# Kernel optimization log

Hardware: AMD Instinct MI355X
Metric: run time of the kernel (lower is better)

Reference implementation:

```python
import jax, jax.numpy as jnp
import numpy as np
from jax import lax

N = 200; E = 3200; HID = 64; NH = 16; OUT = 2 * HID; CAT = NH * OUT  # CAT = 2048
ALPHA = 0.2


def _gat(h, e_attr, adj, n2n, W, a_s, a_d, a_e, We, concat):
    # edge-feature-aware GAT head: logits from Wh_i, Wh_j and projected node2node feats
    Nn = h.shape[0]
    Wh = h @ W                                       # [N, out]
    ee = ((n2n @ We) @ a_e).reshape(Nn, Nn)          # [N, N] edge-feature term
    logits = jax.nn.leaky_relu((Wh @ a_s)[:, None] + (Wh @ a_d)[None, :] + ee,
                               negative_slope=ALPHA)
    logits = jnp.where(adj > 0, logits, -1e9)        # mask to graph structure
    att = jax.nn.softmax(logits, axis=1)
    h2 = att @ Wh
    if concat:
        h2 = jax.nn.elu(h2)
    return h2, jax.nn.elu(e_attr @ We)               # updated node + edge features


def _edge_pool(x, eidx, e, w, b):
    # static-shape edge pooling: score edges, gate nodes by mean incident score
    src, dst = eidx[0], eidx[1]
    s = jax.nn.sigmoid(jnp.concatenate([x[src], x[dst], e], axis=1) @ w + b)  # [E]
    deg = jax.ops.segment_sum(jnp.ones_like(s), src, num_segments=x.shape[0])
    ns = jax.ops.segment_sum(s, src, num_segments=x.shape[0]) / (deg + 1e-6)
    return x * ns[:, None], e * s[:, None]


def _gpool(x, w, b):
    # GlobalAttention: gate_nn = Linear+Sigmoid, softmax over nodes, weighted sum
    gate = jax.nn.softmax(jax.nn.sigmoid(x @ w + b), axis=0)  # [N, 1]
    return jnp.sum(gate * x, axis=0, keepdims=True)           # [1, D]


def _adj_n2n(Nn, eidx, eattr):
    # vectorized version of the per-edge Python loop in _get_adj_node2node
    src, dst = eidx[0], eidx[1]
    adj = jnp.zeros((Nn, Nn), eattr.dtype).at[src, dst].set(1.0)
    n2n = jnp.zeros((Nn * Nn, eattr.shape[1]), eattr.dtype).at[src * Nn + dst].set(eattr)
    return adj, n2n


def _lstm_dir(x, Wih, Whh, b):
    # one LSTM direction over seq x [T, Din] (PyTorch i,f,g,o gate order)
    Hh = Whh.shape[1]
    def step(carry, xt):
        h, c = carry
        g = xt @ Wih.T + h @ Whh.T + b
        i, f, gg, o = jnp.split(g, 4)
        c = jax.nn.sigmoid(f) * c + jax.nn.sigmoid(i) * jnp.tanh(gg)
        h = jax.nn.sigmoid(o) * jnp.tanh(c)
        return (h, c), h
    (_, _), ys = lax.scan(step, (jnp.zeros(Hh, x.dtype), jnp.zeros(Hh, x.dtype)), x)
    return ys


def setup_inputs():
    key = jax.random.key(0)
    ks = iter(jax.random.split(key, 64))
    def rn(shape, scale=0.05):
        return jax.random.normal(next(ks), shape, jnp.float32) * scale
    inp = {}
    for g in (1, 2):
        eidx = jax.random.randint(next(ks), (2, E), 0, N)
        eattr = rn((E, HID), 1.0)
        adj, n2n = _adj_n2n(N, eidx, eattr)
        inp['features%d' % g] = rn((N, HID), 1.0)
        inp['edge_index%d' % g] = eidx
        inp['edgesAttr%d' % g] = eattr
        inp['adjacency%d' % g] = adj
        inp['node2node%d' % g] = n2n
    inp.update(dict(
        W_h=rn((HID, HID)),
        W_gat=rn((NH, HID, OUT)), a_src=rn((NH, OUT)), a_dst=rn((NH, OUT)),
        a_e=rn((NH, OUT)), We_gat=rn((NH, HID, OUT)),
        W_out=rn((CAT, OUT)), ao_src=rn((OUT,)), ao_dst=rn((OUT,)), ao_e=rn((OUT,)),
        We_out=rn((CAT, OUT)),
        ep1_w=rn((3 * CAT,)), ep1_b=rn(()),
        ep2_w=rn((3 * OUT,)), ep2_b=rn(()),
        g1_w=rn((HID, 1)), g1_b=rn((1,)),
        g2_w=rn((CAT, 1)), g2_b=rn((1,)),
        g3_w=rn((OUT, 1)), g3_b=rn((1,)),
        Wih0=rn((2, 512, 35 * HID)), Whh0=rn((2, 512, 128)), b0=rn((2, 512)),
        Wih1=rn((2, 512, 256)), Whh1=rn((2, 512, 128)), b1=rn((2, 512)),
        fc_w=rn((256, 2)), fc_b=rn((2,)),
    ))
    return inp


def reference(features1, features2, edge_index1, edge_index2, edgesAttr1, edgesAttr2,
              adjacency1, adjacency2, node2node1, node2node2,
              W_h, W_gat, a_src, a_dst, a_e, We_gat,
              W_out, ao_src, ao_dst, ao_e, We_out,
              ep1_w, ep1_b, ep2_w, ep2_b,
              g1_w, g1_b, g2_w, g2_b, g3_w, g3_b,
              Wih0, Whh0, b0, Wih1, Whh1, b1, fc_w, fc_b):
    def graph(feat, eidx, eattr, adj, n2n):
        h = jax.nn.elu(feat @ W_h)                              # SingleNodeAttentionLayer
        hs = [_gpool(h, g1_w, g1_b)]
        outs = [_gat(h, eattr, adj, n2n, W_gat[i], a_src[i], a_dst[i], a_e[i],
                     We_gat[i], True) for i in range(NH)]
        h = jnp.concatenate([o[0] for o in outs], axis=1)       # [N, 2048]
        eattr = jnp.concatenate([o[1] for o in outs], axis=1)   # [E, 2048]
        h, eattr = _edge_pool(h, eidx, eattr, ep1_w, ep1_b)
        hs.append(_gpool(h, g2_w, g2_b))
        adj2, n2n2 = _adj_n2n(h.shape[0], eidx, eattr)          # dense [N*N, 2048]
        h, eattr = _gat(h, eattr, adj2, n2n2, W_out, ao_src, ao_dst, ao_e, We_out, False)
        h, eattr = _edge_pool(h, eidx, eattr, ep2_w, ep2_b)
        hs.append(_gpool(h, g3_w, g3_b))
        return jnp.concatenate(hs, axis=1)                      # [1, 35*HID]

    h1 = graph(features1, edge_index1, edgesAttr1, adjacency1, node2node1)
    h2 = graph(features2, edge_index2, edgesAttr2, adjacency2, node2node2)
    x = jnp.concatenate([h1, h2], axis=0)                       # seq [2, 2240]
    for Wih, Whh, b in ((Wih0, Whh0, b0), (Wih1, Whh1, b1)):
        f = _lstm_dir(x, Wih[0], Whh[0], b[0])
        r = _lstm_dir(x[::-1], Wih[1], Whh[1], b[1])[::-1]
        x = jnp.concatenate([f, r], axis=1)                     # [2, 256]
    logits = x[-1] @ fc_w + fc_b
    return jax.nn.softmax(logits)[None, :]                      # [1, nclass]
```

## Files before the change

kernel.cpp:

```cpp
#include <hip/hip_runtime.h>
#include <math.h>

#define DI static __device__ __forceinline__

DI float eluf(float x){ return x > 0.f ? x : expm1f(x); }
DI float lreluf(float x){ return x > 0.f ? x : 0.2f*x; }
DI float sigmf(float x){ return 1.f/(1.f+expf(-x)); }

typedef unsigned short u16;
typedef unsigned int   u32;
typedef __attribute__((ext_vector_type(8))) short short8_t;
typedef __attribute__((ext_vector_type(4))) float f32x4;

DI u16 bf16rne(float f){
  u32 u = __float_as_uint(f);
  u += 0x7fffu + ((u>>16)&1u);
  return (u16)(u>>16);
}

DI f32x4 bmfma(short8_t a, short8_t b, f32x4 c){
  return __builtin_amdgcn_mfma_f32_16x16x32_bf16(a, b, c, 0, 0, 0);
}

constexpr int N=200, E=3200, HID=64, NH=16, OUTD=128, CAT=2048, SEQD=2240;

constexpr int OH0   = 0;
constexpr int OWH   = OH0 + N*HID;
constexpr int OASN  = OWH + NH*N*OUTD;
constexpr int OADN  = OASN + NH*N;
constexpr int OH1   = OADN + NH*N;
constexpr int OXW1  = OH1 + N*CAT;
constexpr int OXW2  = OXW1 + 256;
constexpr int OEW1  = OXW2 + 256;
constexpr int OS1   = OEW1 + E;
constexpr int ODEG1 = OS1 + E;
constexpr int OSS1  = ODEG1 + 256;
constexpr int ORAW1 = OSS1 + 256;
constexpr int OWH2  = ORAW1 + 256;
constexpr int OAS2  = OWH2 + N*OUTD;
constexpr int OAD2  = OAS2 + 256;
constexpr int OEWV  = OAD2 + 256;
constexpr int OH2B  = OEWV + E;
constexpr int OXS2  = OH2B + N*OUTD;
constexpr int OXD2  = OXS2 + 256;
constexpr int ODEG2 = OXD2 + 256;
constexpr int OSS2  = ODEG2 + 256;
constexpr int ORAW2 = OSS2 + 256;
constexpr int ORAW3 = ORAW2 + 256;
constexpr int PGF   = ORAW3 + 256;
constexpr int GLOBF = 10624;
constexpr int TOTF  = GLOBF + 2*PGF;

__device__ __attribute__((aligned(16))) float G_F[TOTF];
__device__ float G_E2PART[(size_t)4*2*E*OUTD];
__device__ float G_EDOTH[2*NH*E];
__device__ float G_WHHT[2*2*128*512];
__device__ int   G_PIDX[2*N*N];
__device__ __attribute__((aligned(16))) u16 G_WGAT_T[NH*OUTD*HID];
__device__ __attribute__((aligned(16))) u16 G_WOUT_T[OUTD*CAT];
__device__ __attribute__((aligned(16))) u16 G_EATTR_BF[2*E*HID];

DI float* gf(int g){ return G_F + GLOBF + (size_t)g*PGF; }
DI float* gwe_ae(){ return G_F; }
DI float* gv_e(){ return G_F + 1024; }
DI float* gy0(){ return G_F + 3072; }
DI float* gy1(){ return G_F + 3584; }
DI float* gxseq(){ return G_F + 4096; }
DI float* gxg(){ return G_F + 8576; }
DI int*   gpidx(int g){ return G_PIDX + g*N*N; }

struct GraphIn {
  const float *feat, *eattr, *adj, *n2n;
  const int   *eidx;
};

struct Params {
  GraphIn g[2];
  const float *W_h, *W_gat, *a_src, *a_dst, *a_e, *We_gat;
  const float *W_out, *ao_src, *ao_dst, *ao_e, *We_out;
  const float *ep1_w, *ep1_b, *ep2_w, *ep2_b;
  const float *g1_w, *g1_b, *g2_w, *g2_b, *g3_w, *g3_b;
  const float *Wih0, *Whh0, *b0, *Wih1, *Whh1, *b1, *fc_w, *fc_b;
  float *out;
};

constexpr int ZPG  = 2*E + 1024;
constexpr int IB_Z = (2*ZPG+255)/256;
constexpr int IB_C = (2*N*N+255)/256;
constexpr int IB_D = (2*2*512*128)/256;
constexpr int IB_E = (NH*HID+CAT+3)/4;
constexpr int IB_H = (2*N+3)/4;
constexpr int IB_W1 = (NH*OUTD*HID)/256;
constexpr int IB_W2 = (OUTD*CAT)/256;
constexpr int IB_EA = (2*E*HID)/256;
__global__ void k_init(Params P){
  int b = blockIdx.x, tid = threadIdx.x;
  if (b < IB_Z){
    int i = b*256 + tid;
    if (i < 2*ZPG){
      int g = i/ZPG, r = i%ZPG;
      int addr = r<E ? OEW1+r : (r<2*E ? OEWV+(r-E) :
                 (r<2*E+512 ? ODEG1+(r-2*E) : ODEG2+(r-2*E-512)));
      gf(g)[addr] = 0.f;
    }
  } else if (b < IB_Z+IB_C){
    int i = (b-IB_Z)*256 + tid; if (i < 2*N*N) G_PIDX[i] = -1;
  } else if (b < IB_Z+IB_C+IB_D){
    int idx = (b-IB_Z-IB_C)*256 + tid;
    int l = idx >> 17;
    int r = idx & 131071;
    int d = r >> 16;
    int r2 = r & 65535;
    int gate = r2 & 511;
    int k = r2 >> 9;
    const float* Whh = l ? P.Whh1 : P.Whh0;
    G_WHHT[idx] = Whh[((size_t)d*512+gate)*128 + k];
  } else if (b < IB_Z+IB_C+IB_D+IB_E){
    int gid = (b-IB_Z-IB_C-IB_D)*4 + (tid>>6);
    int lane = tid & 63;
    if (gid < NH*HID){
      int h = gid/HID, c = gid%HID;
      const float* W = P.We_gat + (size_t)(h*HID+c)*OUTD;
      const float* a = P.a_e + h*OUTD;
      float acc = 0.f;
      for (int o=lane;o<OUTD;o+=64) acc += W[o]*a[o];
      for (int off=32;off>0;off>>=1) acc += __shfl_down(acc,off);
      if (lane==0) gwe_ae()[gid] = acc;
    } else if (gid < NH*HID+CAT){
      int c = gid - NH*HID;
      const float* W = P.We_out + (size_t)c*OUTD;
      float acc = 0.f;
      for (int o=lane;o<OUTD;o+=64) acc += W[o]*P.ao_e[o];
      for (int off=32;off>0;off>>=1) acc += __shfl_down(acc,off);
      if (lane==0) gv_e()[c] = acc;
    }
  } else if (b < IB_Z+IB_C+IB_D+IB_E+IB_H){
    int unit = (b-IB_Z-IB_C-IB_D-IB_E)*4 + (tid>>6);
    if (unit >= 2*N) return;
    int g = unit / N, n = unit % N, c = tid & 63;
    const float* feat = P.g[g].feat;
    float acc = 0.f;
    for (int k=0;k<HID;k++) acc += feat[n*HID+k]*P.W_h[k*HID+c];
    float v = eluf(acc);
    float* f = gf(g);
    f[OH0 + n*HID + c] = v;
    float r = v*P.g1_w[c];
    for (int off=32;off>0;off>>=1) r += __shfl_down(r,off);
    if (c==0) f[ORAW1+n] = r;
  } else if (b < IB_Z+IB_C+IB_D+IB_E+IB_H+IB_W1){
    int i = (b-(IB_Z+IB_C+IB_D+IB_E+IB_H))*256 + tid;
    int h = i>>13, o = (i>>6)&127, c = i&63;
    G_WGAT_T[i] = bf16rne(P.We_gat[(size_t)(h*HID+c)*OUTD + o]);
  } else if (b < IB_Z+IB_C+IB_D+IB_E+IB_H+IB_W1+IB_W2){
    int i = (b-(IB_Z+IB_C+IB_D+IB_E+IB_H+IB_W1))*256 + tid;
    int n = i>>11, q = i&2047;
    G_WOUT_T[i] = bf16rne(P.We_out[(size_t)q*OUTD + n]);
  } else {
    int i = (b-(IB_Z+IB_C+IB_D+IB_E+IB_H+IB_W1+IB_W2))*256 + tid;
    int g = i >= E*HID ? 1 : 0;
    G_EATTR_BF[i] = bf16rne(P.g[g].eattr[i - g*E*HID]);
  }
}
constexpr int IB_TOT = IB_Z+IB_C+IB_D+IB_E+IB_H+IB_W1+IB_W2+IB_EA;


DI void e2p_body(Params& P, int idx, char* smem){
  int g = idx/400, r2 = idx%400, hg = r2/100, eb = r2%100;
  int tid = threadIdx.x;
  int wave = tid>>6, lane = tid&63, l16 = lane&15, l4 = lane>>4;
  u16* Tlds = (u16*)smem;
  int e0 = eb*32;
  int nt0 = wave*2;
  const u16* ea = G_EATTR_BF + ((size_t)g*E + e0)*HID;
  short8_t af00 = *(const short8_t*)(ea + l16*HID + l4*8);
  short8_t af01 = *(const short8_t*)(ea + l16*HID + 32 + l4*8);
  short8_t af10 = *(const short8_t*)(ea + (16+l16)*HID + l4*8);
  short8_t af11 = *(const short8_t*)(ea + (16+l16)*HID + 32 + l4*8);
  float ew1p0[4] = {0.f,0.f,0.f,0.f}, ewvp0[4] = {0.f,0.f,0.f,0.f};
  float ew1p1[4] = {0.f,0.f,0.f,0.f}, ewvp1[4] = {0.f,0.f,0.f,0.f};
  for (int hh=0; hh<4; hh++){
    int h = hg*4 + hh;
    const u16* Wg = G_WGAT_T + (size_t)h*OUTD*HID;
    #pragma unroll
    for (int nn=0; nn<2; nn++){
      int nt = nt0 + nn;
      const u16* Wgn = Wg + (size_t)(nt*16 + l16)*HID + l4*8;
      short8_t wg0 = *(const short8_t*)Wgn;
      short8_t wg1 = *(const short8_t*)(Wgn + 32);
      f32x4 d0 = {0.f,0.f,0.f,0.f}, d1 = {0.f,0.f,0.f,0.f};
      d0 = bmfma(af00, wg0, d0);
      d1 = bmfma(af10, wg0, d1);
      d0 = bmfma(af01, wg1, d0);
      d1 = bmfma(af11, wg1, d1);
      int qg = h*OUTD + nt*16 + l16;
      float w1 = P.ep1_w[2*CAT + qg];
      float wv = gv_e()[qg];
      int qloc = hh*128 + nt*16 + l16;
      #pragma unroll
      for (int r=0;r<4;r++){
        float v0 = d0[r] > 0.f ? d0[r] : expm1f(d0[r]);
        float v1 = d1[r] > 0.f ? d1[r] : expm1f(d1[r]);
        ew1p0[r] += v0*w1; ewvp0[r] += v0*wv;
        ew1p1[r] += v1*w1; ewvp1[r] += v1*wv;
        int row = l4*4 + r;
        int byt = (row*1024 + qloc*2) ^ ((row&7)<<4);
        *(u16*)((char*)Tlds + byt) = bf16rne(v0);
        *(u16*)((char*)Tlds + byt + 16384) = bf16rne(v1);
      }
    }
  }
  const u16* WoA = G_WOUT_T + (size_t)(wave*32 + l16)*CAT + hg*512 + l4*8;
  const u16* WoB = WoA + 16*CAT;
  short8_t w0a = *(const short8_t*)WoA;
  short8_t w0b = *(const short8_t*)WoB;
  short8_t w1a = *(const short8_t*)(WoA + 32);
  short8_t w1b = *(const short8_t*)(WoB + 32);
  float* f = gf(g);
  #pragma unroll
  for (int r=0;r<4;r++){
    float a0 = ew1p0[r], b0 = ewvp0[r], a1 = ew1p1[r], b1 = ewvp1[r];
    a0 += __shfl_xor(a0,1); b0 += __shfl_xor(b0,1); a1 += __shfl_xor(a1,1); b1 += __shfl_xor(b1,1);
    a0 += __shfl_xor(a0,2); b0 += __shfl_xor(b0,2); a1 += __shfl_xor(a1,2); b1 += __shfl_xor(b1,2);
    a0 += __shfl_xor(a0,4); b0 += __shfl_xor(b0,4); a1 += __shfl_xor(a1,4); b1 += __shfl_xor(b1,4);
    a0 += __shfl_xor(a0,8); b0 += __shfl_xor(b0,8); a1 += __shfl_xor(a1,8); b1 += __shfl_xor(b1,8);
    if (l16==0){
      int e = e0 + l4*4 + r;
      atomicAdd(&f[OEW1+e], a0);
      atomicAdd(&f[OEWV+e], b0);
      atomicAdd(&f[OEW1+e+16], a1);
      atomicAdd(&f[OEWV+e+16], b1);
    }
  }
  __syncthreads();
  f32x4 acc00 = {0.f,0.f,0.f,0.f}, acc01 = {0.f,0.f,0.f,0.f};
  f32x4 acc10 = {0.f,0.f,0.f,0.f}, acc11 = {0.f,0.f,0.f,0.f};
  #pragma unroll
  for (int ks=0; ks<16; ks++){
    short8_t na = w0a, nb = w0b;
    if (ks < 14){
      na = *(const short8_t*)(WoA + (ks+2)*32);
      nb = *(const short8_t*)(WoB + (ks+2)*32);
    }
    int byt = (l16*1024 + ks*64 + l4*16) ^ ((l16&7)<<4);
    short8_t a0 = *(const short8_t*)((const char*)Tlds + byt);
    short8_t a1 = *(const short8_t*)((const char*)Tlds + byt + 16384);
    acc00 = bmfma(a0, w0a, acc00);
    acc10 = bmfma(a1, w0a, acc10);
    acc01 = bmfma(a0, w0b, acc01);
    acc11 = bmfma(a1, w0b, acc11);
    w0a = w1a; w0b = w1b; w1a = na; w1b = nb;
  }
  float* dst = G_E2PART + (((size_t)hg*2 + g)*E + e0)*OUTD;
  #pragma unroll
  for (int r=0;r<4;r++){
    int ee = l4*4 + r;
    dst[(size_t)ee*OUTD + wave*32 + l16]      = acc00[r];
    dst[(size_t)ee*OUTD + wave*32 + 16 + l16] = acc01[r];
    dst[(size_t)(16+ee)*OUTD + wave*32 + l16]      = acc10[r];
    dst[(size_t)(16+ee)*OUTD + wave*32 + 16 + l16] = acc11[r];
  }
}

DI void edoth_body(Params& P, int idx, float* s){
  int tid = threadIdx.x;
  int g = idx / (E/16);
  int e0 = (idx % (E/16)) * 16;
  float (*ea)[HID+1] = (float(*)[HID+1])s;
  float (*wa)[HID+1] = (float(*)[HID+1])(s + 16*(HID+1));
  {
    int row = tid >> 4, c0 = (tid & 15)*4;
    float4 v = *(const float4*)&P.g[g].eattr[(size_t)(e0+row)*HID + c0];
    ea[row][c0]=v.x; ea[row][c0+1]=v.y; ea[row][c0+2]=v.z; ea[row][c0+3]=v.w;
    float4 w = *(const float4*)&gwe_ae()[row*HID + c0];
    wa[row][c0]=w.x; wa[row][c0+1]=w.y; wa[row][c0+2]=w.z; wa[row][c0+3]=w.w;
  }
  __syncthreads();
  int h = tid >> 4, el = tid & 15;
  float acc = 0.f;
  #pragma unroll
  for (int c=0;c<HID;c++) acc += ea[el][c]*wa[h][c];
  G_EDOTH[((size_t)g*NH + h)*E + e0 + el] = acc;
}

DI void wh_body(Params& P, int idx, float* s){
  int o = threadIdx.x;
  if (o >= 128) return;
  int g = idx / (N*(NH+1));
  int r = idx % (N*(NH+1));
  int h = r / N, n = r % N;
  float* f = gf(g);
  if (h == NH){
    if (n != 0) return;
    float* att = s;
    float* sb  = s + 200;
    for (int j = o; j < N; j += 128) att[j] = sigmf(f[ORAW1+j] + P.g1_b[0]);
    __syncthreads();
    float m = -3e38f;
    for (int j = o; j < N; j += 128) m = fmaxf(m, att[j]);
    sb[o] = m; __syncthreads();
    for (int sft=64;sft>0;sft>>=1){ if (o<sft) sb[o]=fmaxf(sb[o],sb[o+sft]); __syncthreads(); }
    m = sb[0]; __syncthreads();
    float ss = 0.f;
    for (int j = o; j < N; j += 128){ float e = expf(att[j]-m); ss += e; }
    sb[o] = ss; __syncthreads();
    for (int sft=64;sft>0;sft>>=1){ if (o<sft) sb[o]+=sb[o+sft]; __syncthreads(); }
    float inv = 1.f/sb[0]; __syncthreads();
    for (int j = o; j < N; j += 128) att[j] = expf(att[j]-m)*inv;
    __syncthreads();
    if (o < HID){
      float acc = 0.f;
      for (int j=0;j<N;j++) acc += att[j]*f[OH0 + j*HID + o];
      gxseq()[g*SEQD + o] = acc;
    }
    return;
  }
  float* hs   = s;
  float* sred = s + 64;
  float* dred = s + 192;
  if (o < HID) hs[o] = f[OH0 + n*HID + o];
  __syncthreads();
  const float* W = P.W_gat + (size_t)h*HID*OUTD + o;
  float acc = 0.f;
  for (int c=0;c<HID;c++) acc += hs[c]*W[(size_t)c*OUTD];
  f[OWH + ((size_t)h*N + n)*OUTD + o] = acc;
  sred[o] = acc*P.a_src[h*OUTD+o];
  dred[o] = acc*P.a_dst[h*OUTD+o];
  __syncthreads();
  for (int sft=64;sft>0;sft>>=1){ if (o<sft){ sred[o]+=sred[o+sft]; dred[o]+=dred[o+sft]; } __syncthreads(); }
  if (o==0){ f[OASN+h*N+n]=sred[0]; f[OADN+h*N+n]=dred[0]; }
}

DI void pairs_body(Params& P, int idx){
  int g = idx / 13;
  int e = (idx % 13)*256 + threadIdx.x;
  if (e >= E) return;
  const int* ei = P.g[g].eidx;
  atomicMax(&gpidx(g)[ei[e]*N + ei[E+e]], e);
}

constexpr int MB_E2P = 800, MB_ED = 400, MB_WH = 2*N*(NH+1), MB_PR = 26;
__global__ __launch_bounds__(256) void k_mega(Params P){
  __shared__ __attribute__((aligned(16))) char smem[32768];
  int b = blockIdx.x;
  if (b < MB_E2P) e2p_body(P, b, smem);
  else if (b < MB_E2P+MB_ED) edoth_body(P, b-MB_E2P, (float*)smem);
  else if (b < MB_E2P+MB_ED+MB_WH) wh_body(P, b-(MB_E2P+MB_ED), (float*)smem);
  else pairs_body(P, b-(MB_E2P+MB_ED+MB_WH));
}

__global__ void k_att1(Params P){
  int nb = blockIdx.x, h = blockIdx.y, g = blockIdx.z, tid = threadIdx.x;
  int n0 = nb*4;
  __shared__ float z[4][N];
  __shared__ float red[128];
  __shared__ float sinv[4];
  float* f = gf(g);
  const float* adj = P.g[g].adj;
  const int* pidx = gpidx(g);
  const float* edoth = G_EDOTH + ((size_t)g*NH + h)*E;
  const float* adn = f + OADN + h*N;
  for (int i=0;i<4;i++){
    float asn = f[OASN + h*N + n0+i];
    for (int j = tid; j < N; j += 128){
      float a = adj[(n0+i)*N + j];
      float zz;
      if (a > 0.f){
        int p = pidx[(n0+i)*N + j];
        float ee = (p >= 0) ? edoth[p] : 0.f;
        zz = lreluf(asn + adn[j] + ee);
      } else zz = -1e9f;
      z[i][j] = zz;
    }
  }
  __syncthreads();
  for (int i=0;i<4;i++){
    float m = -3e38f;
    for (int j = tid; j < N; j += 128) m = fmaxf(m, z[i][j]);
    red[tid] = m; __syncthreads();
    for (int s=64;s>0;s>>=1){ if (tid<s) red[tid]=fmaxf(red[tid],red[tid+s]); __syncthreads(); }
    m = red[0]; __syncthreads();
    float ssum = 0.f;
    for (int j = tid; j < N; j += 128){ float e = expf(z[i][j]-m); z[i][j]=e; ssum += e; }
    red[tid] = ssum; __syncthreads();
    for (int s=64;s>0;s>>=1){ if (tid<s) red[tid]+=red[tid+s]; __syncthreads(); }
    if (tid==0) sinv[i] = 1.f/red[0];
    __syncthreads();
  }
  const float* wh = f + OWH + (size_t)h*N*OUTD;
  float a0=0.f,a1=0.f,a2=0.f,a3=0.f;
  for (int j=0;j<N;j++){
    float w = wh[(size_t)j*OUTD + tid];
    a0 += z[0][j]*w; a1 += z[1][j]*w; a2 += z[2][j]*w; a3 += z[3][j]*w;
  }
  f[OH1 + (size_t)(n0+0)*CAT + h*OUTD + tid] = eluf(a0*sinv[0]);
  f[OH1 + (size_t)(n0+1)*CAT + h*OUTD + tid] = eluf(a1*sinv[1]);
  f[OH1 + (size_t)(n0+2)*CAT + h*OUTD + tid] = eluf(a2*sinv[2]);
  f[OH1 + (size_t)(n0+3)*CAT + h*OUTD + tid] = eluf(a3*sinv[3]);
}

__global__ void k_xw1(Params P){
  int n = blockIdx.x, g = blockIdx.y, tid = threadIdx.x;
  __shared__ float s1b[256], s2b[256], s3b[256];
  float* f = gf(g);
  const float* x = f + OH1 + (size_t)n*CAT;
  float a1 = 0.f, a2 = 0.f, a3 = 0.f;
  for (int c = tid; c < CAT; c += 256){
    float xv = x[c];
    a1 += xv*P.ep1_w[c];
    a2 += xv*P.ep1_w[CAT+c];
    a3 += xv*P.g2_w[c];
  }
  s1b[tid]=a1; s2b[tid]=a2; s3b[tid]=a3; __syncthreads();
  for (int s=128;s>0;s>>=1){
    if (tid<s){ s1b[tid]+=s1b[tid+s]; s2b[tid]+=s2b[tid+s]; s3b[tid]+=s3b[tid+s]; }
    __syncthreads();
  }
  if (tid==0){ f[OXW1+n]=s1b[0]; f[OXW2+n]=s2b[0]; f[ORAW2+n]=s3b[0]; }
}

__global__ void k_s1(Params P){
  int e = blockIdx.x*256 + threadIdx.x, g = blockIdx.y;
  if (e >= E) return;
  float* f = gf(g);
  const int* ei = P.g[g].eidx;
  int s = ei[e], d = ei[E+e];
  float v = sigmf(f[OXW1+s] + f[OXW2+d] + f[OEW1+e] + P.ep1_b[0]);
  f[OS1+e] = v;
  atomicAdd(&f[OSS1+s], v);
  atomicAdd(&f[ODEG1+s], 1.f);
}

DI void gpool_body(Params& P, int xoff, int D, int odeg, int rawoff,
                   const float* bb, int outoff, int cb, int g,
                   float* att, float* sb){
  int tid = threadIdx.x;
  float* f = gf(g);
  if (tid < N){
    float sc = f[odeg+256+tid]/(f[odeg+tid]+1e-6f);
    att[tid] = sigmf(f[rawoff+tid]*sc + bb[0]);
  }
  __syncthreads();
  float m = (tid < N) ? att[tid] : -3e38f;
  sb[tid] = m; __syncthreads();
  for (int s=256;s>0;s>>=1){ if (tid<s) sb[tid]=fmaxf(sb[tid],sb[tid+s]); __syncthreads(); }
  m = sb[0]; __syncthreads();
  float e = (tid < N) ? expf(att[tid]-m) : 0.f;
  sb[tid] = e; __syncthreads();
  for (int s=256;s>0;s>>=1){ if (tid<s) sb[tid]+=sb[tid+s]; __syncthreads(); }
  float inv = 1.f/sb[0]; __syncthreads();
  if (tid < N){
    float sc = f[odeg+256+tid]/(f[odeg+tid]+1e-6f);
    att[tid] = e*inv*sc;
  }
  __syncthreads();
  int c = cb*512 + tid;
  if (c < D){
    const float* x = f + xoff;
    float acc = 0.f;
    for (int n=0;n<N;n++) acc += att[n]*x[(size_t)n*D + c];
    gxseq()[g*SEQD + outoff + c] = acc;
  }
}

__global__ void k_gpools(Params P){
  __shared__ float att[N];
  __shared__ float sb[512];
  int b = blockIdx.x;
  if (b < 8){
    int g = b >> 2, cb = b & 3;
    gpool_body(P, OH1, CAT, ODEG1, ORAW2, P.g2_b, HID, cb, g, att, sb);
  } else {
    int g = b - 8;
    gpool_body(P, OH2B, OUTD, ODEG2, ORAW3, P.g3_b, HID+CAT, 0, g, att, sb);
  }
}

__global__ void k_Wh2(Params P){
  int n = blockIdx.x, g = blockIdx.y, tid = threadIdx.x;
  int kq = tid >> 7, o = tid & 127;
  __shared__ float hrow[4][128];
  __shared__ float part[4][128];
  __shared__ float sr[128], dr[128];
  float* f = gf(g);
  const float* x = f + OH1 + (size_t)n*CAT;
  float acc = 0.f;
  for (int cc=0; cc<4; cc++){
    int c0 = kq*512 + cc*128;
    __syncthreads();
    hrow[kq][o] = x[c0 + o];
    __syncthreads();
    const float* W = P.W_out + (size_t)c0*OUTD + o;
    for (int j=0;j<128;j++) acc += hrow[kq][j]*W[(size_t)j*OUTD];
  }
  part[kq][o] = acc;
  __syncthreads();
  if (kq==0){
    float ns = f[OSS1+n]/(f[ODEG1+n]+1e-6f);
    float a = part[0][o]+part[1][o]+part[2][o]+part[3][o];
    float v = a*ns;
    f[OWH2 + (size_t)n*OUTD + o] = v;
    sr[o] = v*P.ao_src[o];
    dr[o] = v*P.ao_dst[o];
  }
  __syncthreads();
  for (int s=64;s>0;s>>=1){
    if (tid<s){ sr[tid]+=sr[tid+s]; dr[tid]+=dr[tid+s]; }
    __syncthreads();
  }
  if (tid==0){ f[OAS2+n]=sr[0]; f[OAD2+n]=dr[0]; }
}

__global__ void k_att2(Params P){
  int n = blockIdx.x, g = blockIdx.y, tid = threadIdx.x;
  __shared__ float z[N];
  __shared__ float red[128];
  __shared__ float dred[128];
  __shared__ float gred[128];
  float* f = gf(g);
  const float* adj = P.g[g].adj;
  const int* pidx = gpidx(g);
  float asn = f[OAS2+n];
  const float* adn = f + OAD2;
  for (int j = tid; j < N; j += 128){
    float a = adj[n*N + j];
    float zz;
    if (a > 0.f){
      int p = pidx[n*N + j];
      float ee = (p >= 0) ? f[OEWV+p]*f[OS1+p] : 0.f;
      zz = lreluf(asn + adn[j] + ee);
    } else zz = -1e9f;
    z[j] = zz;
  }
  __syncthreads();
  float m = -3e38f;
  for (int j = tid; j < N; j += 128) m = fmaxf(m, z[j]);
  red[tid] = m; __syncthreads();
  for (int s=64;s>0;s>>=1){ if (tid<s) red[tid]=fmaxf(red[tid],red[tid+s]); __syncthreads(); }
  m = red[0]; __syncthreads();
  float ssum = 0.f;
  for (int j = tid; j < N; j += 128){ float e = expf(z[j]-m); z[j]=e; ssum += e; }
  red[tid] = ssum; __syncthreads();
  for (int s=64;s>0;s>>=1){ if (tid<s) red[tid]+=red[tid+s]; __syncthreads(); }
  float inv = 1.f/red[0]; __syncthreads();
  const float* wh = f + OWH2;
  float acc = 0.f;
  for (int j=0;j<N;j++){
    float w = z[j];
    if (w != 0.f) acc += w * wh[(size_t)j*OUTD + tid];
  }
  float v = acc*inv;
  f[OH2B + (size_t)n*OUTD + tid] = v;
  red[tid]  = v*P.ep2_w[tid];
  dred[tid] = v*P.ep2_w[OUTD+tid];
  gred[tid] = v*P.g3_w[tid];
  __syncthreads();
  for (int s=64;s>0;s>>=1){
    if (tid<s){ red[tid]+=red[tid+s]; dred[tid]+=dred[tid+s]; gred[tid]+=gred[tid+s]; }
    __syncthreads();
  }
  if (tid==0){ f[OXS2+n]=red[0]; f[OXD2+n]=dred[0]; f[ORAW3+n]=gred[0]; }
}

constexpr int TE2 = 16;
__global__ void k_ew2fin(Params P){
  int e0 = blockIdx.x*TE2, g = blockIdx.y, tid = threadIdx.x;
  __shared__ float lred[2][TE2];
  float* f = gf(g);
  float w2 = P.ep2_w[2*OUTD + tid];
  int lane = tid & 63, wvi = tid >> 6;
  for (int e=0;e<TE2;e++){
    const float* src = G_E2PART + ((size_t)g*E + e0 + e)*OUTD + tid;
    float a = 0.f;
    #pragma unroll
    for (int h=0;h<4;h++) a += src[(size_t)h*2*E*OUTD];
    float v = eluf(f[OS1+e0+e]*a) * w2;
    for (int off=32;off>0;off>>=1) v += __shfl_down(v,off);
    if (lane==0) lred[wvi][e]=v;
  }
  __syncthreads();
  if (tid < TE2){
    int e = e0 + tid;
    float ew2 = lred[0][tid]+lred[1][tid];
    const int* ei = P.g[g].eidx;
    int s = ei[e], d = ei[E+e];
    float v = sigmf(f[OXS2+s] + f[OXD2+d] + ew2 + P.ep2_b[0]);
    atomicAdd(&f[OSS2+s], v);
    atomicAdd(&f[ODEG2+s], 1.f);
  }
}

__global__ void k_lstm_xg(Params P, int layer){
  int gid = blockIdx.x*4 + (threadIdx.x>>6);
  int lane = threadIdx.x & 63;
  int t = gid >> 10;
  int rem = gid & 1023;
  int d = rem >> 9;
  int gate = rem & 511;
  const float* Wih = layer ? P.Wih1 : P.Wih0;
  const float* bb  = layer ? P.b1   : P.b0;
  const float* xin = layer ? gy0()  : gxseq();
  int Din = layer ? 256 : SEQD;
  const float* x = xin + t*Din;
  const float* Wr = Wih + ((size_t)d*512 + gate)*Din;
  float acc = 0.f;
  for (int k=lane; k<Din; k+=64) acc += x[k]*Wr[k];
  for (int off=32; off>0; off>>=1) acc += __shfl_down(acc, off);
  if (lane==0) gxg()[(t*2 + d)*512 + gate] = acc + bb[d*512 + gate];
}

__global__ void k_lstm_rec(Params P, int layer){
  int d = blockIdx.x, tid = threadIdx.x;
  float* yout = layer ? gy1() : gy0();
  const float* T = G_WHHT + (size_t)(layer*2 + d)*128*512;
  __shared__ float h[128], c[128], gbuf[512];
  if (tid < 128){ h[tid]=0.f; c[tid]=0.f; }
  __syncthreads();
  for (int s=0;s<2;s++){
    int t = (d==0) ? s : 1-s;
    float acc = gxg()[(t*2 + d)*512 + tid];
    for (int k=0;k<128;k++) acc += h[k]*T[(size_t)k*512 + tid];
    gbuf[tid] = acc;
    __syncthreads();
    if (tid < 128){
      float ii = sigmf(gbuf[tid]);
      float ff = sigmf(gbuf[128+tid]);
      float gg = tanhf(gbuf[256+tid]);
      float oo = sigmf(gbuf[384+tid]);
      float cn = ff*c[tid] + ii*gg;
      c[tid] = cn;
      float hn = oo*tanhf(cn);
      h[tid] = hn;
      yout[t*256 + d*128 + tid] = hn;
    }
    __syncthreads();
  }
}

__global__ void k_final(Params P){
  int tid = threadIdx.x;
  __shared__ float sb[256], sb2[256];
  const float* x = gy1() + 256;
  sb[tid]  = x[tid]*P.fc_w[tid*2+0];
  sb2[tid] = x[tid]*P.fc_w[tid*2+1];
  __syncthreads();
  for (int s=128;s>0;s>>=1){ if (tid<s){ sb[tid]+=sb[tid+s]; sb2[tid]+=sb2[tid+s]; } __syncthreads(); }
  if (tid==0){
    float l0 = sb[0] + P.fc_b[0];
    float l1 = sb2[0] + P.fc_b[1];
    float m = fmaxf(l0,l1);
    float e0 = expf(l0-m), e1 = expf(l1-m), inv = 1.f/(e0+e1);
    P.out[0] = e0*inv;
    P.out[1] = e1*inv;
  }
}

extern "C" void kernel_launch(void* const* d_in, const int* in_sizes, int n_in,
                              void* d_out, int out_size, void* d_ws, size_t ws_size,
                              hipStream_t stream){
  Params P;
  for (int g=0; g<2; ++g){
    int b = g*5;
    P.g[g].feat  = (const float*)d_in[b+0];
    P.g[g].eidx  = (const int*)d_in[b+1];
    P.g[g].eattr = (const float*)d_in[b+2];
    P.g[g].adj   = (const float*)d_in[b+3];
    P.g[g].n2n   = (const float*)d_in[b+4];
  }
  P.W_h   = (const float*)d_in[10];
  P.W_gat = (const float*)d_in[11];
  P.a_src = (const float*)d_in[12];
  P.a_dst = (const float*)d_in[13];
  P.a_e   = (const float*)d_in[14];
  P.We_gat= (const float*)d_in[15];
  P.W_out = (const float*)d_in[16];
  P.ao_src= (const float*)d_in[17];
  P.ao_dst= (const float*)d_in[18];
  P.ao_e  = (const float*)d_in[19];
  P.We_out= (const float*)d_in[20];
  P.ep1_w = (const float*)d_in[21];
  P.ep1_b = (const float*)d_in[22];
  P.ep2_w = (const float*)d_in[23];
  P.ep2_b = (const float*)d_in[24];
  P.g1_w  = (const float*)d_in[25];
  P.g1_b  = (const float*)d_in[26];
  P.g2_w  = (const float*)d_in[27];
  P.g2_b  = (const float*)d_in[28];
  P.g3_w  = (const float*)d_in[29];
  P.g3_b  = (const float*)d_in[30];
  P.Wih0  = (const float*)d_in[31];
  P.Whh0  = (const float*)d_in[32];
  P.b0    = (const float*)d_in[33];
  P.Wih1  = (const float*)d_in[34];
  P.Whh1  = (const float*)d_in[35];
  P.b1    = (const float*)d_in[36];
  P.fc_w  = (const float*)d_in[37];
  P.fc_b  = (const float*)d_in[38];
  P.out   = (float*)d_out;

  k_init <<<dim3(IB_TOT), 256, 0, stream>>>(P);
  k_mega <<<dim3(MB_E2P+MB_ED+MB_WH+MB_PR), 256, 0, stream>>>(P);
  k_att1 <<<dim3(N/4,NH,2),128, 0, stream>>>(P);
  k_xw1  <<<dim3(N,2),    256, 0, stream>>>(P);
  k_s1   <<<dim3((E+255)/256,2), 256, 0, stream>>>(P);
  k_Wh2  <<<dim3(N,2),    512, 0, stream>>>(P);
  k_att2 <<<dim3(N,2),    128, 0, stream>>>(P);
  k_ew2fin<<<dim3(E/TE2,2),128, 0, stream>>>(P);
  k_gpools<<<dim3(10),    512, 0, stream>>>(P);

  k_lstm_xg <<<dim3(512), 256, 0, stream>>>(P, 0);
  k_lstm_rec<<<dim3(2),   512, 0, stream>>>(P, 0);
  k_lstm_xg <<<dim3(512), 256, 0, stream>>>(P, 1);
  k_lstm_rec<<<dim3(2),   512, 0, stream>>>(P, 1);
  k_final<<<dim3(1), 256, 0, stream>>>(P);
}
```

Measured before the change: 338.3 us.

## Fuse post-attention stages into fewer kernels and merge LSTM layer-1 with final FC

Folds the per-node projection reductions (k_xw1) into the attention kernel's epilogue, accumulated with atomics into zeroed buffers. Merges the s1 edge scoring with a 4-node-per-block Wh2 projection, and att2 with the first global pool. It also moves the node-score scaling algebraically from Wh2 into att2, and fuses the second LSTM recurrence with the final FC/softmax into one 1024-thread block. The aim is to cut launch count and serial kernel boundaries in a latency-bound pipeline, at the cost of atomics and larger shared-memory blocks.

```diff
diff --git a/kernel.cpp b/kernel.cpp
--- a/kernel.cpp
+++ b/kernel.cpp
@@ -84,7 +84,7 @@
   float *out;
 };
 
-constexpr int ZPG  = 2*E + 1024;
+constexpr int ZPG  = 2*E + 1024 + 768;
 constexpr int IB_Z = (2*ZPG+255)/256;
 constexpr int IB_C = (2*N*N+255)/256;
 constexpr int IB_D = (2*2*512*128)/256;
@@ -99,8 +99,14 @@
     int i = b*256 + tid;
     if (i < 2*ZPG){
       int g = i/ZPG, r = i%ZPG;
-      int addr = r<E ? OEW1+r : (r<2*E ? OEWV+(r-E) :
-                 (r<2*E+512 ? ODEG1+(r-2*E) : ODEG2+(r-2*E-512)));
+      int addr;
+      if (r < E) addr = OEW1+r;
+      else if (r < 2*E) addr = OEWV+(r-E);
+      else if (r < 2*E+512) addr = ODEG1+(r-2*E);
+      else if (r < 2*E+1024) addr = ODEG2+(r-2*E-512);
+      else if (r < 2*E+1280) addr = OXW1+(r-2*E-1024);
+      else if (r < 2*E+1536) addr = OXW2+(r-2*E-1280);
+      else addr = ORAW2+(r-2*E-1536);
       gf(g)[addr] = 0.f;
     }
   } else if (b < IB_Z+IB_C){
@@ -354,6 +360,7 @@
   __shared__ float z[4][N];
   __shared__ float red[128];
   __shared__ float sinv[4];
+  __shared__ float lxr[2][12];
   float* f = gf(g);
   const float* adj = P.g[g].adj;
   const int* pidx = gpidx(g);
@@ -392,34 +399,99 @@
     float w = wh[(size_t)j*OUTD + tid];
     a0 += z[0][j]*w; a1 += z[1][j]*w; a2 += z[2][j]*w; a3 += z[3][j]*w;
   }
-  f[OH1 + (size_t)(n0+0)*CAT + h*OUTD + tid] = eluf(a0*sinv[0]);
-  f[OH1 + (size_t)(n0+1)*CAT + h*OUTD + tid] = eluf(a1*sinv[1]);
-  f[OH1 + (size_t)(n0+2)*CAT + h*OUTD + tid] = eluf(a2*sinv[2]);
-  f[OH1 + (size_t)(n0+3)*CAT + h*OUTD + tid] = eluf(a3*sinv[3]);
-}
-
-__global__ void k_xw1(Params P){
-  int n = blockIdx.x, g = blockIdx.y, tid = threadIdx.x;
-  __shared__ float s1b[256], s2b[256], s3b[256];
+  float v0 = eluf(a0*sinv[0]);
+  float v1 = eluf(a1*sinv[1]);
+  float v2 = eluf(a2*sinv[2]);
+  float v3 = eluf(a3*sinv[3]);
+  f[OH1 + (size_t)(n0+0)*CAT + h*OUTD + tid] = v0;
+  f[OH1 + (size_t)(n0+1)*CAT + h*OUTD + tid] = v1;
+  f[OH1 + (size_t)(n0+2)*CAT + h*OUTD + tid] = v2;
+  f[OH1 + (size_t)(n0+3)*CAT + h*OUTD + tid] = v3;
+  float w1 = P.ep1_w[h*OUTD + tid];
+  float w2 = P.ep1_w[CAT + h*OUTD + tid];
+  float w3 = P.g2_w[h*OUTD + tid];
+  float pp[12];
+  pp[0]=v0*w1; pp[1]=v0*w2; pp[2]=v0*w3;
+  pp[3]=v1*w1; pp[4]=v1*w2; pp[5]=v1*w3;
+  pp[6]=v2*w1; pp[7]=v2*w2; pp[8]=v2*w3;
+  pp[9]=v3*w1; pp[10]=v3*w2; pp[11]=v3*w3;
+  #pragma unroll
+  for (int k=0;k<12;k++){
+    #pragma unroll
+    for (int off=32;off>0;off>>=1) pp[k] += __shfl_down(pp[k],off);
+  }
+  int wv = tid>>6, ln = tid&63;
+  if (ln==0){
+    #pragma unroll
+    for (int k=0;k<12;k++) lxr[wv][k]=pp[k];
+  }
+  __syncthreads();
+  if (tid<12){
+    float s = lxr[0][tid]+lxr[1][tid];
+    int node = n0 + tid/3, kind = tid%3;
+    int base = kind==0 ? OXW1 : (kind==1 ? OXW2 : ORAW2);
+    atomicAdd(&f[base + node], s);
+  }
+}
+
+DI void wh2_body(Params& P, int nq, int g, char* smem){
+  float* hrow = (float*)smem;
+  float* part = (float*)(smem + 32768);
+  float* lred = (float*)(smem + 32768 + 8192);
+  int tid = threadIdx.x;
   float* f = gf(g);
-  const float* x = f + OH1 + (size_t)n*CAT;
-  float a1 = 0.f, a2 = 0.f, a3 = 0.f;
-  for (int c = tid; c < CAT; c += 256){
-    float xv = x[c];
-    a1 += xv*P.ep1_w[c];
-    a2 += xv*P.ep1_w[CAT+c];
-    a3 += xv*P.g2_w[c];
-  }
-  s1b[tid]=a1; s2b[tid]=a2; s3b[tid]=a3; __syncthreads();
-  for (int s=128;s>0;s>>=1){
-    if (tid<s){ s1b[tid]+=s1b[tid+s]; s2b[tid]+=s2b[tid+s]; s3b[tid]+=s3b[tid+s]; }
-    __syncthreads();
-  }
-  if (tid==0){ f[OXW1+n]=s1b[0]; f[OXW2+n]=s2b[0]; f[ORAW2+n]=s3b[0]; }
-}
-
-__global__ void k_s1(Params P){
-  int e = blockIdx.x*256 + threadIdx.x, g = blockIdx.y;
+  int n0 = nq*4;
+  for (int idx=tid; idx<4*CAT; idx+=512)
+    hrow[idx] = f[OH1 + (size_t)(n0 + (idx>>11))*CAT + (idx&2047)];
+  __syncthreads();
+  int o = tid&127, kq = tid>>7;
+  float acc0=0.f, acc1=0.f, acc2=0.f, acc3=0.f;
+  const float* W = P.W_out + (size_t)(kq*512)*OUTD + o;
+  const float* hA = hrow + kq*512;
+  const float* hB = hA + CAT;
+  const float* hC = hB + CAT;
+  const float* hD = hC + CAT;
+  for (int j=0;j<512;j++){
+    float w = W[(size_t)j*OUTD];
+    acc0 += hA[j]*w; acc1 += hB[j]*w; acc2 += hC[j]*w; acc3 += hD[j]*w;
+  }
+  part[(kq*4+0)*128+o]=acc0;
+  part[(kq*4+1)*128+o]=acc1;
+  part[(kq*4+2)*128+o]=acc2;
+  part[(kq*4+3)*128+o]=acc3;
+  __syncthreads();
+  float a[4];
+  #pragma unroll
+  for (int i=0;i<4;i++)
+    a[i] = part[(0*4+i)*128+o]+part[(1*4+i)*128+o]+part[(2*4+i)*128+o]+part[(3*4+i)*128+o];
+  if (kq==0){
+    #pragma unroll
+    for (int i=0;i<4;i++) f[OWH2 + (size_t)(n0+i)*OUTD + o] = a[i];
+  }
+  float pr[8];
+  #pragma unroll
+  for (int i=0;i<4;i++){ pr[i*2] = a[i]*P.ao_src[o]; pr[i*2+1] = a[i]*P.ao_dst[o]; }
+  #pragma unroll
+  for (int k=0;k<8;k++){
+    #pragma unroll
+    for (int off=32;off>0;off>>=1) pr[k] += __shfl_down(pr[k],off);
+  }
+  int wv = tid>>6, ln = tid&63;
+  if (wv<2 && ln==0){
+    #pragma unroll
+    for (int k=0;k<8;k++) lred[wv*8+k]=pr[k];
+  }
+  __syncthreads();
+  if (tid<8){
+    float s = lred[tid]+lred[8+tid];
+    int node = n0 + (tid>>1);
+    if (tid&1) f[OAD2+node]=s; else f[OAS2+node]=s;
+  }
+}
+
+DI void s1_body(Params& P, int idx){
+  int g = idx/7;
+  int e = (idx%7)*512 + threadIdx.x;
   if (e >= E) return;
   float* f = gf(g);
   const int* ei = P.g[g].eidx;
@@ -428,6 +500,13 @@
   f[OS1+e] = v;
   atomicAdd(&f[OSS1+s], v);
   atomicAdd(&f[ODEG1+s], 1.f);
+}
+
+__global__ __launch_bounds__(512) void k_s1wh2(Params P){
+  __shared__ __attribute__((aligned(16))) char smem[32768 + 8192 + 64];
+  int b = blockIdx.x;
+  if (b < 100) wh2_body(P, b>>1, b&1, smem);
+  else s1_body(P, b-100);
 }
 
 DI void gpool_body(Params& P, int xoff, int D, int odeg, int rawoff,
@@ -462,103 +541,84 @@
   }
 }
 
-__global__ void k_gpools(Params P){
-  __shared__ float att[N];
-  __shared__ float sb[512];
-  int b = blockIdx.x;
-  if (b < 8){
-    int g = b >> 2, cb = b & 3;
-    gpool_body(P, OH1, CAT, ODEG1, ORAW2, P.g2_b, HID, cb, g, att, sb);
-  } else {
-    int g = b - 8;
-    gpool_body(P, OH2B, OUTD, ODEG2, ORAW3, P.g3_b, HID+CAT, 0, g, att, sb);
-  }
-}
-
-__global__ void k_Wh2(Params P){
-  int n = blockIdx.x, g = blockIdx.y, tid = threadIdx.x;
-  int kq = tid >> 7, o = tid & 127;
-  __shared__ float hrow[4][128];
-  __shared__ float part[4][128];
-  __shared__ float sr[128], dr[128];
-  float* f = gf(g);
-  const float* x = f + OH1 + (size_t)n*CAT;
-  float acc = 0.f;
-  for (int cc=0; cc<4; cc++){
-    int c0 = kq*512 + cc*128;
-    __syncthreads();
-    hrow[kq][o] = x[c0 + o];
-    __syncthreads();
-    const float* W = P.W_out + (size_t)c0*OUTD + o;
-    for (int j=0;j<128;j++) acc += hrow[kq][j]*W[(size_t)j*OUTD];
-  }
-  part[kq][o] = acc;
-  __syncthreads();
-  if (kq==0){
-    float ns = f[OSS1+n]/(f[ODEG1+n]+1e-6f);
-    float a = part[0][o]+part[1][o]+part[2][o]+part[3][o];
-    float v = a*ns;
-    f[OWH2 + (size_t)n*OUTD + o] = v;
-    sr[o] = v*P.ao_src[o];
-    dr[o] = v*P.ao_dst[o];
-  }
-  __syncthreads();
-  for (int s=64;s>0;s>>=1){
-    if (tid<s){ sr[tid]+=sr[tid+s]; dr[tid]+=dr[tid+s]; }
-    __syncthreads();
-  }
-  if (tid==0){ f[OAS2+n]=sr[0]; f[OAD2+n]=dr[0]; }
-}
-
-__global__ void k_att2(Params P){
-  int n = blockIdx.x, g = blockIdx.y, tid = threadIdx.x;
-  __shared__ float z[N];
-  __shared__ float red[128];
-  __shared__ float dred[128];
-  __shared__ float gred[128];
+DI void att2_body(Params& P, int nb, int g, char* smem){
+  int tid = threadIdx.x;
+  int grp = tid>>7, o = tid&127;
+  int n0 = nb*4, n = n0 + grp;
+  float (*z)[N] = (float(*)[N])smem;
+  float* nsv = (float*)(smem + 4*N*4);
+  float* red = nsv + 256;
+  float* inv = red + 512;
+  float* lxr = inv + 4;
   float* f = gf(g);
   const float* adj = P.g[g].adj;
   const int* pidx = gpidx(g);
-  float asn = f[OAS2+n];
-  const float* adn = f + OAD2;
-  for (int j = tid; j < N; j += 128){
+  for (int j = tid; j < N; j += 512)
+    nsv[j] = f[OSS1+j]/(f[ODEG1+j]+1e-6f);
+  __syncthreads();
+  float asn = f[OAS2+n]*nsv[n];
+  for (int j = o; j < N; j += 128){
     float a = adj[n*N + j];
     float zz;
     if (a > 0.f){
       int p = pidx[n*N + j];
       float ee = (p >= 0) ? f[OEWV+p]*f[OS1+p] : 0.f;
-      zz = lreluf(asn + adn[j] + ee);
+      zz = lreluf(asn + f[OAD2+j]*nsv[j] + ee);
     } else zz = -1e9f;
-    z[j] = zz;
+    z[grp][j] = zz;
   }
   __syncthreads();
   float m = -3e38f;
-  for (int j = tid; j < N; j += 128) m = fmaxf(m, z[j]);
-  red[tid] = m; __syncthreads();
-  for (int s=64;s>0;s>>=1){ if (tid<s) red[tid]=fmaxf(red[tid],red[tid+s]); __syncthreads(); }
-  m = red[0]; __syncthreads();
+  for (int j = o; j < N; j += 128) m = fmaxf(m, z[grp][j]);
+  red[grp*128+o] = m; __syncthreads();
+  for (int s=64;s>0;s>>=1){ if (o<s) red[grp*128+o]=fmaxf(red[grp*128+o],red[grp*128+o+s]); __syncthreads(); }
+  m = red[grp*128]; __syncthreads();
   float ssum = 0.f;
-  for (int j = tid; j < N; j += 128){ float e = expf(z[j]-m); z[j]=e; ssum += e; }
-  red[tid] = ssum; __syncthreads();
-  for (int s=64;s>0;s>>=1){ if (tid<s) red[tid]+=red[tid+s]; __syncthreads(); }
-  float inv = 1.f/red[0]; __syncthreads();
+  for (int j = o; j < N; j += 128){ float e = expf(z[grp][j]-m); z[grp][j]=e; ssum += e; }
+  red[grp*128+o] = ssum; __syncthreads();
+  for (int s=64;s>0;s>>=1){ if (o<s) red[grp*128+o]+=red[grp*128+o+s]; __syncthreads(); }
+  if (o==0) inv[grp] = 1.f/red[grp*128];
+  __syncthreads();
   const float* wh = f + OWH2;
   float acc = 0.f;
   for (int j=0;j<N;j++){
-    float w = z[j];
-    if (w != 0.f) acc += w * wh[(size_t)j*OUTD + tid];
-  }
-  float v = acc*inv;
-  f[OH2B + (size_t)n*OUTD + tid] = v;
-  red[tid]  = v*P.ep2_w[tid];
-  dred[tid] = v*P.ep2_w[OUTD+tid];
-  gred[tid] = v*P.g3_w[tid];
-  __syncthreads();
-  for (int s=64;s>0;s>>=1){
-    if (tid<s){ red[tid]+=red[tid+s]; dred[tid]+=dred[tid+s]; gred[tid]+=gred[tid+s]; }
-    __syncthreads();
-  }
-  if (tid==0){ f[OXS2+n]=red[0]; f[OXD2+n]=dred[0]; f[ORAW3+n]=gred[0]; }
+    float w = z[grp][j]*nsv[j];
+    if (w != 0.f) acc += w * wh[(size_t)j*OUTD + o];
+  }
+  float v = acc*inv[grp];
+  f[OH2B + (size_t)n*OUTD + o] = v;
+  float pr[3];
+  pr[0] = v*P.ep2_w[o];
+  pr[1] = v*P.ep2_w[OUTD+o];
+  pr[2] = v*P.g3_w[o];
+  #pragma unroll
+  for (int k=0;k<3;k++){
+    #pragma unroll
+    for (int off=32;off>0;off>>=1) pr[k] += __shfl_down(pr[k],off);
+  }
+  int wv = tid>>6, ln = tid&63;
+  if (ln==0){
+    lxr[wv*3+0]=pr[0]; lxr[wv*3+1]=pr[1]; lxr[wv*3+2]=pr[2];
+  }
+  __syncthreads();
+  if (tid<12){
+    int node = tid/3, kind = tid%3;
+    float s = lxr[(node*2)*3+kind] + lxr[(node*2+1)*3+kind];
+    int base = kind==0 ? OXS2 : (kind==1 ? OXD2 : ORAW3);
+    f[base + n0 + node] = s;
+  }
+}
+
+__global__ __launch_bounds__(512) void k_att2p(Params P){
+  __shared__ __attribute__((aligned(16))) char smem[8192];
+  int b = blockIdx.x;
+  if (b < 100) att2_body(P, b>>1, b&1, smem);
+  else {
+    int idx = b-100, g = idx>>2, cb = idx&3;
+    float* att = (float*)smem;
+    float* sb  = att + 256;
+    gpool_body(P, OH1, CAT, ODEG1, ORAW2, P.g2_b, HID, cb, g, att, sb);
+  }
 }
 
 constexpr int TE2 = 16;
@@ -587,6 +647,13 @@
     atomicAdd(&f[OSS2+s], v);
     atomicAdd(&f[ODEG2+s], 1.f);
   }
+}
+
+__global__ __launch_bounds__(512) void k_pool3(Params P){
+  __shared__ float att[256];
+  __shared__ float sb[512];
+  int g = blockIdx.x;
+  gpool_body(P, OH2B, OUTD, ODEG2, ORAW3, P.g3_b, HID+CAT, 0, g, att, sb);
 }
 
 __global__ void k_lstm_xg(Params P, int layer){
@@ -636,14 +703,42 @@
   }
 }
 
-__global__ void k_final(Params P){
+__global__ __launch_bounds__(1024) void k_recfin(Params P){
   int tid = threadIdx.x;
+  int d = tid>>9, gt = tid&511;
+  __shared__ float h[2][128], c[2][128], gbuf[2][512], yfin[256];
   __shared__ float sb[256], sb2[256];
-  const float* x = gy1() + 256;
-  sb[tid]  = x[tid]*P.fc_w[tid*2+0];
-  sb2[tid] = x[tid]*P.fc_w[tid*2+1];
-  __syncthreads();
-  for (int s=128;s>0;s>>=1){ if (tid<s){ sb[tid]+=sb[tid+s]; sb2[tid]+=sb2[tid+s]; } __syncthreads(); }
+  if (gt < 128){ h[d][gt]=0.f; c[d][gt]=0.f; }
+  __syncthreads();
+  const float* T = G_WHHT + (size_t)(2 + d)*128*512;
+  for (int s=0;s<2;s++){
+    int t = (d==0) ? s : 1-s;
+    float acc = gxg()[(t*2 + d)*512 + gt];
+    for (int k=0;k<128;k++) acc += h[d][k]*T[(size_t)k*512 + gt];
+    gbuf[d][gt] = acc;
+    __syncthreads();
+    if (gt < 128){
+      float ii = sigmf(gbuf[d][gt]);
+      float ff = sigmf(gbuf[d][128+gt]);
+      float gg = tanhf(gbuf[d][256+gt]);
+      float oo = sigmf(gbuf[d][384+gt]);
+      float cn = ff*c[d][gt] + ii*gg;
+      c[d][gt] = cn;
+      float hn = oo*tanhf(cn);
+      h[d][gt] = hn;
+      if (t==1) yfin[d*128 + gt] = hn;
+    }
+    __syncthreads();
+  }
+  if (tid < 256){
+    sb[tid]  = yfin[tid]*P.fc_w[tid*2+0];
+    sb2[tid] = yfin[tid]*P.fc_w[tid*2+1];
+  }
+  __syncthreads();
+  for (int s=128;s>0;s>>=1){
+    if (tid<s){ sb[tid]+=sb[tid+s]; sb2[tid]+=sb2[tid+s]; }
+    __syncthreads();
+  }
   if (tid==0){
     float l0 = sb[0] + P.fc_b[0];
     float l1 = sb2[0] + P.fc_b[1];
@@ -700,16 +795,12 @@
   k_init <<<dim3(IB_TOT), 256, 0, stream>>>(P);
   k_mega <<<dim3(MB_E2P+MB_ED+MB_WH+MB_PR), 256, 0, stream>>>(P);
   k_att1 <<<dim3(N/4,NH,2),128, 0, stream>>>(P);
-  k_xw1  <<<dim3(N,2),    256, 0, stream>>>(P);
-  k_s1   <<<dim3((E+255)/256,2), 256, 0, stream>>>(P);
-  k_Wh2  <<<dim3(N,2),    512, 0, stream>>>(P);
-  k_att2 <<<dim3(N,2),    128, 0, stream>>>(P);
+  k_s1wh2<<<dim3(114),    512, 0, stream>>>(P);
+  k_att2p<<<dim3(108),    512, 0, stream>>>(P);
   k_ew2fin<<<dim3(E/TE2,2),128, 0, stream>>>(P);
-  k_gpools<<<dim3(10),    512, 0, stream>>>(P);
-
+  k_pool3<<<dim3(2),      512, 0, stream>>>(P);
   k_lstm_xg <<<dim3(512), 256, 0, stream>>>(P, 0);
   k_lstm_rec<<<dim3(2),   512, 0, stream>>>(P, 0);
   k_lstm_xg <<<dim3(512), 256, 0, stream>>>(P, 1);
-  k_lstm_rec<<<dim3(2),   512, 0, stream>>>(P, 1);
-  k_final<<<dim3(1), 256, 0, stream>>>(P);
-}
+  k_recfin<<<dim3(1),    1024, 0, stream>>>(P);
+}
```

Measured after the change: 345.5 us. 1.02x slower.
